# Performance work log

Hardware: AMD Instinct MI355X
Metric: run time of the kernel (lower is better)

The kernel has to match this reference:

```python
import jax, jax.numpy as jnp
import numpy as np

T, D, F, E, K, R = 4096, 1024, 4096, 8, 2, 16
SCALE = 32.0 / 16.0  # lora_alpha / lora_rank


def setup_inputs() -> dict:
    key = jax.random.key(0)
    ks = jax.random.split(key, 11)
    rn = lambda k, shape, sc: jax.random.normal(k, shape, dtype=jnp.float32) * sc
    return {
        "x": rn(ks[0], (T, D), 1.0),
        "gate_w": rn(ks[1], (E, D), 0.02),   # router gate_.weight
        "W1": rn(ks[2], (F, D), 0.02),       # gate_proj (base)
        "W3": rn(ks[3], (F, D), 0.02),       # up_proj (base)
        "W2": rn(ks[4], (D, F), 0.02),       # down_proj (base)
        "A1": rn(ks[5], (E, R, D), 0.02),    # per-expert LoRA A for gate_proj
        "B1": rn(ks[6], (E, F, R), 0.02),
        "A3": rn(ks[7], (E, R, D), 0.02),    # per-expert LoRA A for up_proj
        "B3": rn(ks[8], (E, F, R), 0.02),
        "A2": rn(ks[9], (E, R, F), 0.02),    # per-expert LoRA A for down_proj
        "B2": rn(ks[10], (E, D, R), 0.02),
    }


def reference(x, gate_w, W1, W3, W2, A1, B1, A3, B3, A2, B2):
    # Router: logits -> softmax -> top-k -> renormalize (Mixtral/MixLoRA style)
    router_logits = x @ gate_w.T                      # [T, E]
    probs = jax.nn.softmax(router_logits, axis=-1)
    topv, topi = jax.lax.top_k(probs, K)              # [T, K]
    topv = topv / jnp.sum(topv, axis=-1, keepdims=True)
    tok = jnp.arange(x.shape[0])
    route = jnp.zeros_like(probs).at[tok[:, None], topi].set(topv)  # [T, E] sparse weights

    # Shared base projections computed once (experts share base weights, differ by LoRA)
    xg = x @ W1.T                                     # [T, F]
    xu = x @ W3.T                                     # [T, F]

    out = jnp.zeros_like(x)
    for e in range(E):  # fixed small expert count; not a data-dim loop
        g = xg + SCALE * ((x @ A1[e].T) @ B1[e].T)    # gate_proj + LoRA
        u = xu + SCALE * ((x @ A3[e].T) @ B3[e].T)    # up_proj + LoRA
        h = jax.nn.silu(g) * u                        # SwiGLU
        y = h @ W2.T + SCALE * ((h @ A2[e].T) @ B2[e].T)  # down_proj + LoRA
        out = out + route[:, e:e + 1] * y             # weighted scatter-add combine
    return out, router_logits
```

## Files before the change

kernel.cpp:

```cpp
#include <hip/hip_runtime.h>
#include <stdint.h>

#define T_ 4096
#define D_ 1024
#define F_ 4096
#define E_ 8
#define NCAT 8448
#define KH 4224
#define NTILE_MAX 320

typedef __attribute__((ext_vector_type(8))) short          s16x8;
typedef __attribute__((ext_vector_type(8))) unsigned short u16x8;
typedef __attribute__((ext_vector_type(4))) unsigned short u16x4;
typedef __attribute__((ext_vector_type(4))) float          f32x4;

__device__ __forceinline__ unsigned short f2bf(float f) {
  unsigned u = __float_as_uint(f);
  u += 0x7fffu + ((u >> 16) & 1u);
  return (unsigned short)(u >> 16);
}
__device__ __forceinline__ float b2f(unsigned short h) {
  return __uint_as_float(((unsigned)h) << 16);
}

__device__ __forceinline__ void cvt8(const float* __restrict__ s, unsigned short* __restrict__ d) {
  float4 a = *(const float4*)s;
  float4 b = *(const float4*)(s + 4);
  u16x8 v;
  v[0] = f2bf(a.x); v[1] = f2bf(a.y); v[2] = f2bf(a.z); v[3] = f2bf(a.w);
  v[4] = f2bf(b.x); v[5] = f2bf(b.y); v[6] = f2bf(b.z); v[7] = f2bf(b.w);
  *(u16x8*)d = v;
}
__device__ __forceinline__ void cvt8s2(const float* __restrict__ s, unsigned short* __restrict__ d) {
  float4 a = *(const float4*)s;
  float4 b = *(const float4*)(s + 4);
  u16x8 v;
  v[0] = f2bf(2.f * a.x); v[1] = f2bf(2.f * a.y); v[2] = f2bf(2.f * a.z); v[3] = f2bf(2.f * a.w);
  v[4] = f2bf(2.f * b.x); v[5] = f2bf(2.f * b.y); v[6] = f2bf(2.f * b.z); v[7] = f2bf(2.f * b.w);
  *(u16x8*)d = v;
}

__global__ __launch_bounds__(256) void conv_kernel(
    const float* __restrict__ x,  const float* __restrict__ W1,
    const float* __restrict__ W3, const float* __restrict__ W2,
    const float* __restrict__ A1, const float* __restrict__ A3,
    const float* __restrict__ B1, const float* __restrict__ B3,
    const float* __restrict__ A2, const float* __restrict__ B2,
    unsigned short* __restrict__ xb,  unsigned short* __restrict__ Wcatb,
    unsigned short* __restrict__ W2cat, unsigned short* __restrict__ B1b,
    unsigned short* __restrict__ B3b, unsigned short* __restrict__ A2r) {
  const int y = blockIdx.y;
  const size_t i0 = ((size_t)blockIdx.x * 256 + threadIdx.x) * 8;
  if (y == 0) { cvt8(x + i0, xb + i0); }
  else if (y == 1) {
    const size_t d = i0 >> 12, f = i0 & 4095;
    cvt8(W2 + i0, W2cat + d * KH + f);
  }
  else if (y == 2) { cvt8(W1 + i0, Wcatb + i0); }
  else if (y == 3) { cvt8(W3 + i0, Wcatb + 4194304 + i0); }
  else {
    const size_t o8 = (size_t)blockIdx.x * 256 + threadIdx.x;
    if (o8 < 245760) {
      const size_t o = o8 * 8;
      if (o < 131072)        cvt8s2(A1 + o, Wcatb + 8388608 + o);
      else if (o < 262144)   cvt8s2(A3 + (o - 131072), Wcatb + 8388608 + o);
      else if (o < 786432)   cvt8(B1 + (o - 262144), B1b + (o - 262144));
      else if (o < 1310720)  cvt8(B3 + (o - 786432), B3b + (o - 786432));
      else if (o < 1835008)  cvt8s2(A2 + (o - 1310720), A2r + (o - 1310720));
      else {
        const size_t oo = o - 1835008;
        const size_t d = oo >> 7, j = oo & 127;
        const size_t e = j >> 4, r0 = j & 15;
        cvt8(B2 + e * ((size_t)D_ * 16) + d * 16 + r0, W2cat + d * KH + 4096 + j);
      }
    }
  }
}

__global__ __launch_bounds__(256) void router_kernel(
    const float* __restrict__ x, const float* __restrict__ gw,
    float* __restrict__ logits, int2* __restrict__ topi, float2* __restrict__ topw) {
  const int wave = threadIdx.x >> 6, lane = threadIdx.x & 63;
  const int t = blockIdx.x * 4 + wave;
  const float* xr = x + (size_t)t * D_;
  float acc[E_] = {0, 0, 0, 0, 0, 0, 0, 0};
  for (int it = 0; it < 16; ++it) {
    const int d = lane + it * 64;
    const float xv = xr[d];
#pragma unroll
    for (int e = 0; e < E_; ++e) acc[e] += xv * gw[e * D_ + d];
  }
#pragma unroll
  for (int e = 0; e < E_; ++e)
#pragma unroll
    for (int m = 1; m < 64; m <<= 1) acc[e] += __shfl_xor(acc[e], m);
  if (lane == 0) {
    float m0v = acc[0]; int m0i = 0;
#pragma unroll
    for (int e = 1; e < E_; ++e) if (acc[e] > m0v) { m0v = acc[e]; m0i = e; }
    float m1v = -3.0e38f; int m1i = 0;
#pragma unroll
    for (int e = 0; e < E_; ++e) if (e != m0i && acc[e] > m1v) { m1v = acc[e]; m1i = e; }
    const float e1 = __expf(m1v - m0v);
    const float inv = 1.f / (1.f + e1);
    topi[t] = make_int2(m0i, m1i);
    topw[t] = make_float2(inv, e1 * inv);
#pragma unroll
    for (int e = 0; e < E_; ++e) logits[(size_t)t * E_ + e] = acc[e];
  }
}

__global__ __launch_bounds__(256) void bucket_kernel(
    const int2* __restrict__ topi, int* __restrict__ bucketTok, int* __restrict__ bucketCnt) {
  const int pid = blockIdx.x;
  const int e0 = pid >> 3, e1 = pid & 7;
  __shared__ int cnt;
  if (threadIdx.x == 0) cnt = 0;
  __syncthreads();
  for (int t = threadIdx.x; t < T_; t += 256) {
    const int2 ti = topi[t];
    if (ti.x == e0 && ti.y == e1) {
      const int s = atomicAdd(&cnt, 1);
      bucketTok[pid * T_ + s] = t;
    }
  }
  __syncthreads();
  if (threadIdx.x == 0) bucketCnt[pid] = cnt;
}

__global__ void tilelist_kernel(const int* __restrict__ bucketCnt, int* __restrict__ tileList) {
  const int pid = threadIdx.x;
  const int ntile = (bucketCnt[pid] + 15) >> 4;
  int scan = ntile;
#pragma unroll
  for (int m = 1; m < 64; m <<= 1) {
    const int v = __shfl_up(scan, m);
    if (pid >= m) scan += v;
  }
  const int base = scan - ntile;
  const int total = __shfl(scan, 63);
  for (int i = 0; i < ntile; ++i) tileList[base + i] = (pid << 16) | i;
  for (int i = total + pid; i < NTILE_MAX; i += 64) tileList[i] = -1;
}

__device__ __forceinline__ void cstore(float* C, size_t i, float v) { C[i] = v; }
__device__ __forceinline__ void cstore(unsigned short* C, size_t i, float v) { C[i] = f2bf(v); }

#define GLL(g, l) __builtin_amdgcn_global_load_lds(                            \
    (const __attribute__((address_space(1))) void*)(g),                       \
    (__attribute__((address_space(3))) void*)(l), 16, 0, 0)

template <int BN, typename OUT_T>
__global__ __launch_bounds__(256) void gemm_bt(
    const unsigned short* __restrict__ A, const unsigned short* __restrict__ B,
    OUT_T* __restrict__ C, int M, int N, int K, int nbx) {
  constexpr int WCOL = BN / 2, NF = WCOL / 16;
  constexpr int BITER = BN / 32;
  __shared__ __align__(16) char As[2 * 16384];
  __shared__ __align__(16) char Bs[2 * BN * 128];
  const int tid = threadIdx.x;
  int bid = blockIdx.x;
  bid = (bid & 7) * (gridDim.x >> 3) + (bid >> 3);
  const int bx = bid % nbx, by = bid / nbx;
  const long m0 = (long)bx * 128, n0 = (long)by * BN;

  const unsigned short* asrc[4];
  const unsigned short* bsrc[BITER];
#pragma unroll
  for (int i = 0; i < 4; ++i) {
    const int g = i * 256 + tid, row = g >> 3, cb = (g & 7) ^ (row & 7);
    asrc[i] = A + (m0 + row) * (size_t)K + cb * 8;
  }
#pragma unroll
  for (int i = 0; i < BITER; ++i) {
    const int g = i * 256 + tid, row = g >> 3, cb = (g & 7) ^ (row & 7);
    bsrc[i] = B + (n0 + row) * (size_t)K + cb * 8;
  }
  const int lane = tid & 63, wave = tid >> 6;
  const int wr = wave >> 1, wc = wave & 1;
  const int wb = (tid & 192) * 16;
  int aoff[4][2], boff[NF][2];
#pragma unroll
  for (int mf = 0; mf < 4; ++mf) {
    const int ra = wr * 64 + mf * 16 + (lane & 15);
#pragma unroll
    for (int ks = 0; ks < 2; ++ks) {
      const int kb = (ks * 32 + (lane >> 4) * 8) * 2;
      aoff[mf][ks] = (ra * 128 + kb) ^ ((ra & 7) << 4);
    }
  }
#pragma unroll
  for (int nf = 0; nf < NF; ++nf) {
    const int rb = wc * WCOL + nf * 16 + (lane & 15);
#pragma unroll
    for (int ks = 0; ks < 2; ++ks) {
      const int kb = (ks * 32 + (lane >> 4) * 8) * 2;
      boff[nf][ks] = (rb * 128 + kb) ^ ((rb & 7) << 4);
    }
  }

  auto STAGE = [&](int buf, int kt) {
    const size_t ko = (size_t)kt * 64;
#pragma unroll
    for (int i = 0; i < 4; ++i) GLL(asrc[i] + ko, As + buf * 16384 + i * 4096 + wb);
#pragma unroll
    for (int i = 0; i < BITER; ++i) GLL(bsrc[i] + ko, Bs + buf * (BN * 128) + i * 4096 + wb);
  };

  f32x4 acc[4][NF] = {};
  const int nk = K >> 6;
  int cur = 0;
  STAGE(0, 0);
  asm volatile("s_waitcnt vmcnt(0)" ::: "memory");
  __builtin_amdgcn_s_barrier();
  for (int kt = 0; kt < nk; ++kt) {
    if (kt + 1 < nk) STAGE(cur ^ 1, kt + 1);
    const char* Ab = As + cur * 16384;
    const char* Bb = Bs + cur * (BN * 128);
#pragma unroll
    for (int ks = 0; ks < 2; ++ks) {
      s16x8 af[4], bfv[NF];
#pragma unroll
      for (int mf = 0; mf < 4; ++mf) af[mf] = *(const s16x8*)(Ab + aoff[mf][ks]);
#pragma unroll
      for (int nf = 0; nf < NF; ++nf) bfv[nf] = *(const s16x8*)(Bb + boff[nf][ks]);
#pragma unroll
      for (int mf = 0; mf < 4; ++mf)
#pragma unroll
        for (int nf = 0; nf < NF; ++nf)
          acc[mf][nf] = __builtin_amdgcn_mfma_f32_16x16x32_bf16(af[mf], bfv[nf], acc[mf][nf], 0, 0, 0);
    }
    asm volatile("s_waitcnt vmcnt(0)" ::: "memory");
    __builtin_amdgcn_s_barrier();
    cur ^= 1;
  }
#pragma unroll
  for (int mf = 0; mf < 4; ++mf) {
    const int row0 = (int)m0 + wr * 64 + mf * 16 + ((lane >> 4) << 2);
#pragma unroll
    for (int nf = 0; nf < NF; ++nf) {
      const long col = n0 + wc * WCOL + nf * 16 + (lane & 15);
#pragma unroll
      for (int q = 0; q < 4; ++q)
        cstore(C, (size_t)(row0 + q) * N + col, acc[mf][nf][q]);
    }
  }
}

__global__ __launch_bounds__(256) void s3d_kernel(
    const unsigned short* __restrict__ xguP,
    const unsigned short* __restrict__ B1b,
    const unsigned short* __restrict__ B3b,
    const unsigned short* __restrict__ A2r,
    const int* __restrict__ bucketTok, const int* __restrict__ bucketCnt,
    const float2* __restrict__ topw, const int* __restrict__ tileList,
    unsigned short* __restrict__ hq,
    float* __restrict__ Qpart) {
  const int entry = tileList[blockIdx.x];
  if (entry < 0) return;
  const int pid = entry >> 16, z = entry & 0xffff;
  const int nt = bucketCnt[pid];
  const int e0 = pid >> 3, e1 = pid & 7;

  __shared__ int   ldsTok[16];
  __shared__ float ldsW[2][16];
  __shared__ __align__(16) unsigned short hwT[4][2][16][40];
  const int tid = threadIdx.x;
  if (tid < 16) {
    int s = z * 16 + tid; if (s >= nt) s = nt - 1;
    const int t = bucketTok[pid * T_ + s];
    ldsTok[tid] = t;
    const float2 w = topw[t];
    ldsW[0][tid] = w.x; ldsW[1][tid] = w.y;
  }
  __syncthreads();

  const int lane = tid & 63, wave = tid >> 6;
  const int col = lane & 15, chunk = lane >> 4;

  const int t = ldsTok[col];
  const float w0 = ldsW[0][col], w1 = ldsW[1][col];
  const unsigned short* abase = xguP + (size_t)t * NCAT + 8192 +
                                (chunk >> 1) * 128 + (chunk & 1) * 8;
  const s16x8 afrag0 = *(const s16x8*)(abase + e0 * 16);
  const s16x8 afrag1 = *(const s16x8*)(abase + e1 * 16);

  unsigned short (*hw_w)[16][40] = hwT[wave];
  f32x4 qacc0 = {}, qacc1 = {};
  const int ft0 = blockIdx.y * 64 + wave * 16;

  for (int p = 0; p < 8; ++p) {
#pragma unroll
    for (int half = 0; half < 2; ++half) {
      const int i = p * 2 + half;
      const int fcol = (ft0 + i) * 16 + col;
      s16x8 bg0 = {}, bu0 = {}, bg1 = {}, bu1 = {};
      if (chunk < 2) {
        bg0 = *(const s16x8*)(B1b + ((size_t)e0 * F_ + fcol) * 16 + chunk * 8);
        bg1 = *(const s16x8*)(B1b + ((size_t)e1 * F_ + fcol) * 16 + chunk * 8);
      } else {
        bu0 = *(const s16x8*)(B3b + ((size_t)e0 * F_ + fcol) * 16 + (chunk - 2) * 8);
        bu1 = *(const s16x8*)(B3b + ((size_t)e1 * F_ + fcol) * 16 + (chunk - 2) * 8);
      }
      f32x4 accg0 = {}, accu0 = {}, accg1 = {}, accu1 = {};
      accg0 = __builtin_amdgcn_mfma_f32_16x16x32_bf16(bg0, afrag0, accg0, 0, 0, 0);
      accu0 = __builtin_amdgcn_mfma_f32_16x16x32_bf16(bu0, afrag0, accu0, 0, 0, 0);
      accg1 = __builtin_amdgcn_mfma_f32_16x16x32_bf16(bg1, afrag1, accg1, 0, 0, 0);
      accu1 = __builtin_amdgcn_mfma_f32_16x16x32_bf16(bu1, afrag1, accu1, 0, 0, 0);

      const int fbase = (ft0 + i) * 16 + chunk * 4;
      const u16x4 xgv = *(const u16x4*)(xguP + (size_t)t * NCAT + fbase);
      const u16x4 xuv = *(const u16x4*)(xguP + (size_t)t * NCAT + 4096 + fbase);
      u16x4 hqv, h0v, h1v;
#pragma unroll
      for (int q = 0; q < 4; ++q) {
        const float xg = b2f(xgv[q]);
        const float xu = b2f(xuv[q]);
        const float g0 = xg + accg0[q], u0 = xu + accu0[q];
        const float g1 = xg + accg1[q], u1 = xu + accu1[q];
        const float h0 = (g0 / (1.f + __expf(-g0))) * u0;
        const float h1 = (g1 / (1.f + __expf(-g1))) * u1;
        const unsigned short hb0 = f2bf(w0 * h0);
        const unsigned short hb1 = f2bf(w1 * h1);
        h0v[q] = hb0; h1v[q] = hb1;
        hqv[q] = f2bf(b2f(hb0) + b2f(hb1));
      }
      *(u16x4*)(hq + (size_t)t * KH + fbase) = hqv;
      *(u16x4*)&hw_w[0][col][half * 16 + chunk * 4] = h0v;
      *(u16x4*)&hw_w[1][col][half * 16 + chunk * 4] = h1v;
    }
    asm volatile("s_waitcnt lgkmcnt(0)" ::: "memory");
    const s16x8 hf0 = *(const s16x8*)&hw_w[0][lane & 15][(lane >> 4) * 8];
    const s16x8 hf1 = *(const s16x8*)&hw_w[1][lane & 15][(lane >> 4) * 8];
    const int fb = (ft0 + 2 * p) * 16 + (lane >> 4) * 8;
    const s16x8 a2f0 = *(const s16x8*)(A2r + ((size_t)e0 * 16 + (lane & 15)) * F_ + fb);
    const s16x8 a2f1 = *(const s16x8*)(A2r + ((size_t)e1 * 16 + (lane & 15)) * F_ + fb);
    qacc0 = __builtin_amdgcn_mfma_f32_16x16x32_bf16(hf0, a2f0, qacc0, 0, 0, 0);
    qacc1 = __builtin_amdgcn_mfma_f32_16x16x32_bf16(hf1, a2f1, qacc1, 0, 0, 0);
  }

  const int r = lane & 15;
  float* qp = Qpart + ((size_t)blockIdx.y * 4 + wave) * T_ * 32;
#pragma unroll
  for (int q = 0; q < 4; ++q) {
    const int tq = ldsTok[chunk * 4 + q];
    qp[(size_t)tq * 32 + r]      = qacc0[q];
    qp[(size_t)tq * 32 + 16 + r] = qacc1[q];
  }
}

__global__ __launch_bounds__(256) void qscatter_kernel(
    const float* __restrict__ Qpart, const int2* __restrict__ topi,
    unsigned short* __restrict__ hq) {
  const int gid = blockIdx.x * 256 + threadIdx.x;
  const int t = gid >> 7, j = gid & 127;
  const int2 ti = topi[t];
  const int eb = j >> 4, r = j & 15;
  float v = 0.f;
  if (eb == ti.x) {
#pragma unroll
    for (int st = 0; st < 16; ++st) v += Qpart[(size_t)st * (T_ * 32) + t * 32 + r];
  } else if (eb == ti.y) {
#pragma unroll
    for (int st = 0; st < 16; ++st) v += Qpart[(size_t)st * (T_ * 32) + t * 32 + 16 + r];
  }
  hq[(size_t)t * KH + 4096 + j] = f2bf(v);
}

extern "C" void kernel_launch(void* const* d_in, const int* in_sizes, int n_in,
                              void* d_out, int out_size, void* d_ws, size_t ws_size,
                              hipStream_t stream) {
  (void)in_sizes; (void)n_in; (void)out_size; (void)ws_size;
  const float* x   = (const float*)d_in[0];
  const float* gw  = (const float*)d_in[1];
  const float* W1  = (const float*)d_in[2];
  const float* W3  = (const float*)d_in[3];
  const float* W2  = (const float*)d_in[4];
  const float* A1  = (const float*)d_in[5];
  const float* B1  = (const float*)d_in[6];
  const float* A3  = (const float*)d_in[7];
  const float* B3  = (const float*)d_in[8];
  const float* A2  = (const float*)d_in[9];
  const float* B2  = (const float*)d_in[10];
  float* out = (float*)d_out;
  float* logits = out + (size_t)T_ * D_;

  char* w = (char*)d_ws;
  auto alloc = [&](size_t bytes) { char* p = w; w += (bytes + 255) & ~(size_t)255; return p; };
  unsigned short* xb    = (unsigned short*)alloc((size_t)T_ * D_ * 2);
  unsigned short* Wcatb = (unsigned short*)alloc((size_t)NCAT * D_ * 2);
  unsigned short* W2cat = (unsigned short*)alloc((size_t)D_ * KH * 2);
  unsigned short* B1b   = (unsigned short*)alloc((size_t)E_ * F_ * 16 * 2);
  unsigned short* B3b   = (unsigned short*)alloc((size_t)E_ * F_ * 16 * 2);
  unsigned short* A2r   = (unsigned short*)alloc((size_t)E_ * 16 * F_ * 2);
  unsigned short* xguP  = (unsigned short*)alloc((size_t)T_ * NCAT * 2);
  unsigned short* hq    = (unsigned short*)alloc((size_t)T_ * KH * 2);
  float* Qpart          = (float*)alloc((size_t)16 * T_ * 32 * 4);
  int* bucketTok        = (int*)alloc((size_t)64 * T_ * 4);
  int* bucketCnt        = (int*)alloc((size_t)64 * 4);
  int* tileList         = (int*)alloc((size_t)NTILE_MAX * 4);
  int2* topi            = (int2*)alloc((size_t)T_ * 8);
  float2* topw          = (float2*)alloc((size_t)T_ * 8);

  conv_kernel<<<dim3(2048, 5), 256, 0, stream>>>(x, W1, W3, W2, A1, A3, B1, B3, A2, B2,
                                                 xb, Wcatb, W2cat, B1b, B3b, A2r);
  router_kernel<<<dim3(1024), 256, 0, stream>>>(x, gw, logits, topi, topw);
  bucket_kernel<<<dim3(64), 256, 0, stream>>>(topi, bucketTok, bucketCnt);
  tilelist_kernel<<<dim3(1), 64, 0, stream>>>(bucketCnt, tileList);
  gemm_bt<128, unsigned short><<<dim3(32 * 66), 256, 0, stream>>>(
      xb, Wcatb, xguP, T_, NCAT, 1024, 32);
  s3d_kernel<<<dim3(NTILE_MAX, 4), 256, 0, stream>>>(xguP, B1b, B3b, A2r, bucketTok,
                                                     bucketCnt, topw, tileList, hq, Qpart);
  qscatter_kernel<<<dim3(2048), 256, 0, stream>>>(Qpart, topi, hq);
  gemm_bt<64, float><<<dim3(32 * 16), 256, 0, stream>>>(hq, W2cat, out, T_, D_, KH, 32);
}
```

Baseline: 245.9 us.

## Split-K the down-projection GEMM with a 128-wide tile and add reduction kernel

The final down-projection GEMM moves from a 64-wide N tile over the full K=4224 to a 128-wide tile split into two K halves along blockIdx.z. Each half writes partial fp32 results into the reused xguP workspace, and a new sum2 kernel adds them into the output. This trades one extra launch and a 32 MB partial read/write for larger per-block reuse and the same block count (512). SiLU division is also replaced by a hardware reciprocal multiply in s3d.

Result: faster. 240.1 us, median of 2 (-2.4%).

```diff
diff --git a/kernel.cpp b/kernel.cpp
--- a/kernel.cpp
+++ b/kernel.cpp
@@ -153,7 +153,7 @@
 template <int BN, typename OUT_T>
 __global__ __launch_bounds__(256) void gemm_bt(
     const unsigned short* __restrict__ A, const unsigned short* __restrict__ B,
-    OUT_T* __restrict__ C, int M, int N, int K, int nbx) {
+    OUT_T* __restrict__ C, int M, int N, int Kstride, int ksub, int nbx) {
   constexpr int WCOL = BN / 2, NF = WCOL / 16;
   constexpr int BITER = BN / 32;
   __shared__ __align__(16) char As[2 * 16384];
@@ -163,18 +163,20 @@
   bid = (bid & 7) * (gridDim.x >> 3) + (bid >> 3);
   const int bx = bid % nbx, by = bid / nbx;
   const long m0 = (long)bx * 128, n0 = (long)by * BN;
+  const int k0 = blockIdx.z * ksub;
+  C += (size_t)blockIdx.z * M * N;
 
   const unsigned short* asrc[4];
   const unsigned short* bsrc[BITER];
 #pragma unroll
   for (int i = 0; i < 4; ++i) {
     const int g = i * 256 + tid, row = g >> 3, cb = (g & 7) ^ (row & 7);
-    asrc[i] = A + (m0 + row) * (size_t)K + cb * 8;
+    asrc[i] = A + (m0 + row) * (size_t)Kstride + k0 + cb * 8;
   }
 #pragma unroll
   for (int i = 0; i < BITER; ++i) {
     const int g = i * 256 + tid, row = g >> 3, cb = (g & 7) ^ (row & 7);
-    bsrc[i] = B + (n0 + row) * (size_t)K + cb * 8;
+    bsrc[i] = B + (n0 + row) * (size_t)Kstride + k0 + cb * 8;
   }
   const int lane = tid & 63, wave = tid >> 6;
   const int wr = wave >> 1, wc = wave & 1;
@@ -208,7 +210,7 @@
   };
 
   f32x4 acc[4][NF] = {};
-  const int nk = K >> 6;
+  const int nk = ksub >> 6;
   int cur = 0;
   STAGE(0, 0);
   asm volatile("s_waitcnt vmcnt(0)" ::: "memory");
@@ -318,8 +320,8 @@
         const float xu = b2f(xuv[q]);
         const float g0 = xg + accg0[q], u0 = xu + accu0[q];
         const float g1 = xg + accg1[q], u1 = xu + accu1[q];
-        const float h0 = (g0 / (1.f + __expf(-g0))) * u0;
-        const float h1 = (g1 / (1.f + __expf(-g1))) * u1;
+        const float h0 = g0 * u0 * __builtin_amdgcn_rcpf(1.f + __expf(-g0));
+        const float h1 = g1 * u1 * __builtin_amdgcn_rcpf(1.f + __expf(-g1));
         const unsigned short hb0 = f2bf(w0 * h0);
         const unsigned short hb1 = f2bf(w1 * h1);
         h0v[q] = hb0; h1v[q] = hb1;
@@ -365,6 +367,16 @@
     for (int st = 0; st < 16; ++st) v += Qpart[(size_t)st * (T_ * 32) + t * 32 + 16 + r];
   }
   hq[(size_t)t * KH + 4096 + j] = f2bf(v);
+}
+
+__global__ __launch_bounds__(256) void sum2_kernel(const float* __restrict__ Op,
+                                                   float* __restrict__ out) {
+  const size_t i = ((size_t)blockIdx.x * 256 + threadIdx.x) * 4;
+  const float4 a = *(const float4*)(Op + i);
+  const float4 b = *(const float4*)(Op + (size_t)T_ * D_ + i);
+  float4 o;
+  o.x = a.x + b.x; o.y = a.y + b.y; o.z = a.z + b.z; o.w = a.w + b.w;
+  *(float4*)(out + i) = o;
 }
 
 extern "C" void kernel_launch(void* const* d_in, const int* in_sizes, int n_in,
@@ -401,16 +413,19 @@
   int* tileList         = (int*)alloc((size_t)NTILE_MAX * 4);
   int2* topi            = (int2*)alloc((size_t)T_ * 8);
   float2* topw          = (float2*)alloc((size_t)T_ * 8);
+  float* Opart          = (float*)xguP;
 
   conv_kernel<<<dim3(2048, 5), 256, 0, stream>>>(x, W1, W3, W2, A1, A3, B1, B3, A2, B2,
                                                  xb, Wcatb, W2cat, B1b, B3b, A2r);
   router_kernel<<<dim3(1024), 256, 0, stream>>>(x, gw, logits, topi, topw);
   bucket_kernel<<<dim3(64), 256, 0, stream>>>(topi, bucketTok, bucketCnt);
   tilelist_kernel<<<dim3(1), 64, 0, stream>>>(bucketCnt, tileList);
-  gemm_bt<128, unsigned short><<<dim3(32 * 66), 256, 0, stream>>>(
-      xb, Wcatb, xguP, T_, NCAT, 1024, 32);
+  gemm_bt<128, unsigned short><<<dim3(32 * 66, 1, 1), 256, 0, stream>>>(
+      xb, Wcatb, xguP, T_, NCAT, 1024, 1024, 32);
   s3d_kernel<<<dim3(NTILE_MAX, 4), 256, 0, stream>>>(xguP, B1b, B3b, A2r, bucketTok,
                                                      bucketCnt, topw, tileList, hq, Qpart);
   qscatter_kernel<<<dim3(2048), 256, 0, stream>>>(Qpart, topi, hq);
-  gemm_bt<64, float><<<dim3(32 * 16), 256, 0, stream>>>(hq, W2cat, out, T_, D_, KH, 32);
-}
+  gemm_bt<128, float><<<dim3(32 * 8, 1, 2), 256, 0, stream>>>(
+      hq, W2cat, Opart, T_, D_, KH, 2112, 32);
+  sum2_kernel<<<dim3(4096), 256, 0, stream>>>(Opart, out);
+}
```
